# Kernel optimization log

Hardware: AMD Instinct MI355X
Metric: run time of the kernel (lower is better)

The kernel has to match this reference:

```python
import jax, jax.numpy as jnp
import numpy as np

N_NODES = 100000
N_EDGES = 1600000
IN_C = 64
OUT_C = 64


def setup_inputs() -> dict:
    key = jax.random.key(0)
    k1, k2, k3, k4, k5, k6 = jax.random.split(key, 6)
    x = jax.random.normal(k1, (N_NODES, IN_C), dtype=jnp.float32)
    column_index = jax.random.randint(k2, (N_EDGES,), 0, N_NODES, dtype=jnp.int32)
    row_index = jnp.sort(jax.random.randint(k3, (N_EDGES,), 0, N_NODES, dtype=jnp.int32))
    degrees = jax.random.uniform(k4, (N_NODES,), dtype=jnp.float32)
    # glorot (xavier_uniform) weight init, zero bias, matching reset_parameters()
    limit = np.sqrt(6.0 / (IN_C + OUT_C)).astype(np.float32)
    weight = jax.random.uniform(k5, (IN_C, OUT_C), dtype=jnp.float32, minval=-limit, maxval=limit)
    bias = jnp.zeros((OUT_C,), dtype=jnp.float32)
    return {"x": x, "weight": weight, "bias": bias, "column_index": column_index,
            "row_index": row_index, "degrees": degrees}


def reference(x, weight, bias, column_index, row_index, degrees):
    # GCN: transform then normalized neighbor aggregation (GNNAdvisor / ROF math).
    h = x @ weight                               # [N, out_c]
    gathered = h[column_index]                   # [E, out_c] gather source features
    agg = jax.ops.segment_sum(gathered, row_index, num_segments=N_NODES)  # [N, out_c]
    out = agg * degrees[:, None] + bias          # per-dst degree norm + bias
    return out
```

## Files before the change

kernel.cpp:

```cpp
#include <hip/hip_runtime.h>
#include <hip/hip_bf16.h>

#define IN_C 64
#define OUT_C 64

typedef __attribute__((ext_vector_type(8))) short bf16x8;
typedef __attribute__((ext_vector_type(4))) float f32x4;

__device__ __forceinline__ short f2bf(float f) {
    unsigned u = __float_as_uint(f);
    unsigned r = (u + 0x7FFFu + ((u >> 16) & 1u)) >> 16;
    return (short)r;
}

__global__ __launch_bounds__(256) void gcn_prep_kernel(
    const float* __restrict__ x, const float* __restrict__ w,
    unsigned short* __restrict__ h,
    const int* __restrict__ row, int* __restrict__ rowptr,
    int n_nodes, int n_edges, int gemm_blocks) {
    if ((int)blockIdx.x < gemm_blocks) {
        __shared__ bf16x8 wlds[512];
        const int tid  = threadIdx.x;
        const int lane = tid & 63;
        const int wv   = tid >> 6;
        const int m    = lane & 15;
        const int g    = lane >> 4;

        #pragma unroll
        for (int i = tid; i < IN_C * OUT_C; i += 256) {
            const int k = i >> 6, c = i & 63;
            const int ks = k >> 5, gg = (k >> 3) & 3, j = k & 7;
            const int nt = c >> 4, mm = c & 15;
            ((short*)wlds)[((ks * 4 + nt) * 64 + gg * 16 + mm) * 8 + j] =
                f2bf(w[i]);
        }
        __syncthreads();

        const int node0 = ((int)blockIdx.x * 4 + wv) * 16;
        if (node0 >= n_nodes) return;

        bf16x8 bfr[2][4];
        #pragma unroll
        for (int ks = 0; ks < 2; ++ks) {
            #pragma unroll
            for (int nt = 0; nt < 4; ++nt) {
                bfr[ks][nt] = wlds[(ks * 4 + nt) * 64 + g * 16 + m];
            }
        }

        const int arow = min(node0 + m, n_nodes - 1);
        const float* xr = x + (size_t)arow * IN_C;
        bf16x8 afr[2];
        #pragma unroll
        for (int ks = 0; ks < 2; ++ks) {
            const float4 p0 = *(const float4*)(xr + ks * 32 + g * 8);
            const float4 p1 = *(const float4*)(xr + ks * 32 + g * 8 + 4);
            union { short s[8]; bf16x8 v; } u;
            u.s[0] = f2bf(p0.x); u.s[1] = f2bf(p0.y);
            u.s[2] = f2bf(p0.z); u.s[3] = f2bf(p0.w);
            u.s[4] = f2bf(p1.x); u.s[5] = f2bf(p1.y);
            u.s[6] = f2bf(p1.z); u.s[7] = f2bf(p1.w);
            afr[ks] = u.v;
        }

        f32x4 acc[4];
        #pragma unroll
        for (int nt = 0; nt < 4; ++nt) acc[nt] = (f32x4){0.f, 0.f, 0.f, 0.f};
        #pragma unroll
        for (int ks = 0; ks < 2; ++ks) {
            #pragma unroll
            for (int nt = 0; nt < 4; ++nt) {
                acc[nt] = __builtin_amdgcn_mfma_f32_16x16x32_bf16(
                    afr[ks], bfr[ks][nt], acc[nt], 0, 0, 0);
            }
        }

        #pragma unroll
        for (int j = 0; j < 4; ++j) {
            const int node = node0 + g * 4 + j;
            if (node < n_nodes) {
                #pragma unroll
                for (int nt = 0; nt < 4; ++nt) {
                    h[(size_t)node * OUT_C + nt * 16 + m] =
                        (unsigned short)f2bf(acc[nt][j]);
                }
            }
        }
    } else {
        const int t  = ((int)blockIdx.x - gemm_blocks) * 256 + threadIdx.x;
        const int e0 = t * 4;
        if (e0 >= n_edges) return;
        const int4 r4 = *(const int4*)(row + e0);
        int rprev = (e0 == 0) ? -1 : row[e0 - 1];
        int rr[4] = {r4.x, r4.y, r4.z, r4.w};
        #pragma unroll
        for (int i = 0; i < 4; ++i) {
            if (e0 + i < n_edges) {
                for (int n = rprev + 1; n <= rr[i]; ++n) rowptr[n] = e0 + i;
                rprev = rr[i];
            }
        }
        if (e0 + 4 >= n_edges) {
            for (int n = rprev + 1; n <= n_nodes; ++n) rowptr[n] = n_edges;
        }
    }
}

#define UNPACK_ADD(v)                                   \
    do {                                                \
        acc[0] += __uint_as_float((v).x << 16);         \
        acc[1] += __uint_as_float((v).x & 0xFFFF0000u); \
        acc[2] += __uint_as_float((v).y << 16);         \
        acc[3] += __uint_as_float((v).y & 0xFFFF0000u); \
        acc[4] += __uint_as_float((v).z << 16);         \
        acc[5] += __uint_as_float((v).z & 0xFFFF0000u); \
        acc[6] += __uint_as_float((v).w << 16);         \
        acc[7] += __uint_as_float((v).w & 0xFFFF0000u); \
    } while (0)

__global__ __launch_bounds__(256) void gcn_agg_kernel(
    const uint4* __restrict__ h4, const int* __restrict__ col,
    const int* __restrict__ rowptr, const float* __restrict__ deg,
    const float4* __restrict__ bias4, float4* __restrict__ out4,
    int n_nodes) {
    const int tid  = threadIdx.x;
    const int node = blockIdx.x * 32 + (tid >> 3);
    if (node >= n_nodes) return;
    const int lo   = tid & 7;

    const int begin = rowptr[node];
    const int end   = rowptr[node + 1];
    const int last  = end - 1;

    float acc[8] = {0.f, 0.f, 0.f, 0.f, 0.f, 0.f, 0.f, 0.f};
    for (int e = begin; e < end; e += 8) {
        int c[8];
        #pragma unroll
        for (int i = 0; i < 8; ++i) c[i] = col[min(e + i, last)];
        uint4 v[8];
        #pragma unroll
        for (int i = 0; i < 8; ++i) v[i] = h4[(size_t)c[i] * 8 + lo];
        UNPACK_ADD(v[0]);
        #pragma unroll
        for (int i = 1; i < 8; ++i) {
            if (e + i <= last) UNPACK_ADD(v[i]);
        }
    }

    const float  d  = deg[node];
    const float4 b0 = bias4[lo * 2];
    const float4 b1 = bias4[lo * 2 + 1];
    float4 oa, ob;
    oa.x = fmaf(acc[0], d, b0.x);
    oa.y = fmaf(acc[1], d, b0.y);
    oa.z = fmaf(acc[2], d, b0.z);
    oa.w = fmaf(acc[3], d, b0.w);
    ob.x = fmaf(acc[4], d, b1.x);
    ob.y = fmaf(acc[5], d, b1.y);
    ob.z = fmaf(acc[6], d, b1.z);
    ob.w = fmaf(acc[7], d, b1.w);
    out4[(size_t)node * 16 + lo * 2]     = oa;
    out4[(size_t)node * 16 + lo * 2 + 1] = ob;
}

extern "C" void kernel_launch(void* const* d_in, const int* in_sizes, int n_in,
                              void* d_out, int out_size, void* d_ws, size_t ws_size,
                              hipStream_t stream) {
    const float* x    = (const float*)d_in[0];
    const float* w    = (const float*)d_in[1];
    const float* bias = (const float*)d_in[2];
    const int* col    = (const int*)d_in[3];
    const int* row    = (const int*)d_in[4];
    const float* deg  = (const float*)d_in[5];

    const int n_nodes = in_sizes[5];
    const int n_edges = in_sizes[3];

    unsigned short* h = (unsigned short*)d_ws;
    int* rowptr = (int*)((char*)d_ws +
                         (size_t)n_nodes * OUT_C * sizeof(unsigned short));

    const int gemm_blocks   = (n_nodes + 63) / 64;
    const int rowptr_blocks = (n_edges + 1023) / 1024;
    gcn_prep_kernel<<<gemm_blocks + rowptr_blocks, 256, 0, stream>>>(
        x, w, h, row, rowptr, n_nodes, n_edges, gemm_blocks);

    const int agg_blocks = (n_nodes + 31) / 32;
    gcn_agg_kernel<<<agg_blocks, 256, 0, stream>>>(
        (const uint4*)h, col, rowptr, deg,
        (const float4*)bias, (float4*)d_out, n_nodes);
}
```

Measured before the change: 126.9 us.

## Fuse prep and aggregation into one persistent cooperative kernel with grid sync

Replaces the two-launch sequence (GEMM plus rowptr build, then aggregation) with a single persistent cooperative kernel. It loops over the prep tiles, performs a grid-wide barrier, then loops over the aggregation blocks. Each block stages the weights into LDS once, and the change removes one kernel launch and the gap between kernels. In exchange it caps the grid at 2048 resident blocks, pays the cost of a grid sync and a per-call occupancy query, and falls back to the old two-kernel path if the cooperative launch fails.

```diff
diff --git a/kernel.cpp b/kernel.cpp
--- a/kernel.cpp
+++ b/kernel.cpp
@@ -1,5 +1,7 @@
 #include <hip/hip_runtime.h>
-#include <hip/hip_bf16.h>
+#include <hip/hip_cooperative_groups.h>
+
+namespace cg = cooperative_groups;
 
 #define IN_C 64
 #define OUT_C 64
@@ -11,99 +13,6 @@
     unsigned u = __float_as_uint(f);
     unsigned r = (u + 0x7FFFu + ((u >> 16) & 1u)) >> 16;
     return (short)r;
-}
-
-__global__ __launch_bounds__(256) void gcn_prep_kernel(
-    const float* __restrict__ x, const float* __restrict__ w,
-    unsigned short* __restrict__ h,
-    const int* __restrict__ row, int* __restrict__ rowptr,
-    int n_nodes, int n_edges, int gemm_blocks) {
-    if ((int)blockIdx.x < gemm_blocks) {
-        __shared__ bf16x8 wlds[512];
-        const int tid  = threadIdx.x;
-        const int lane = tid & 63;
-        const int wv   = tid >> 6;
-        const int m    = lane & 15;
-        const int g    = lane >> 4;
-
-        #pragma unroll
-        for (int i = tid; i < IN_C * OUT_C; i += 256) {
-            const int k = i >> 6, c = i & 63;
-            const int ks = k >> 5, gg = (k >> 3) & 3, j = k & 7;
-            const int nt = c >> 4, mm = c & 15;
-            ((short*)wlds)[((ks * 4 + nt) * 64 + gg * 16 + mm) * 8 + j] =
-                f2bf(w[i]);
-        }
-        __syncthreads();
-
-        const int node0 = ((int)blockIdx.x * 4 + wv) * 16;
-        if (node0 >= n_nodes) return;
-
-        bf16x8 bfr[2][4];
-        #pragma unroll
-        for (int ks = 0; ks < 2; ++ks) {
-            #pragma unroll
-            for (int nt = 0; nt < 4; ++nt) {
-                bfr[ks][nt] = wlds[(ks * 4 + nt) * 64 + g * 16 + m];
-            }
-        }
-
-        const int arow = min(node0 + m, n_nodes - 1);
-        const float* xr = x + (size_t)arow * IN_C;
-        bf16x8 afr[2];
-        #pragma unroll
-        for (int ks = 0; ks < 2; ++ks) {
-            const float4 p0 = *(const float4*)(xr + ks * 32 + g * 8);
-            const float4 p1 = *(const float4*)(xr + ks * 32 + g * 8 + 4);
-            union { short s[8]; bf16x8 v; } u;
-            u.s[0] = f2bf(p0.x); u.s[1] = f2bf(p0.y);
-            u.s[2] = f2bf(p0.z); u.s[3] = f2bf(p0.w);
-            u.s[4] = f2bf(p1.x); u.s[5] = f2bf(p1.y);
-            u.s[6] = f2bf(p1.z); u.s[7] = f2bf(p1.w);
-            afr[ks] = u.v;
-        }
-
-        f32x4 acc[4];
-        #pragma unroll
-        for (int nt = 0; nt < 4; ++nt) acc[nt] = (f32x4){0.f, 0.f, 0.f, 0.f};
-        #pragma unroll
-        for (int ks = 0; ks < 2; ++ks) {
-            #pragma unroll
-            for (int nt = 0; nt < 4; ++nt) {
-                acc[nt] = __builtin_amdgcn_mfma_f32_16x16x32_bf16(
-                    afr[ks], bfr[ks][nt], acc[nt], 0, 0, 0);
-            }
-        }
-
-        #pragma unroll
-        for (int j = 0; j < 4; ++j) {
-            const int node = node0 + g * 4 + j;
-            if (node < n_nodes) {
-                #pragma unroll
-                for (int nt = 0; nt < 4; ++nt) {
-                    h[(size_t)node * OUT_C + nt * 16 + m] =
-                        (unsigned short)f2bf(acc[nt][j]);
-                }
-            }
-        }
-    } else {
-        const int t  = ((int)blockIdx.x - gemm_blocks) * 256 + threadIdx.x;
-        const int e0 = t * 4;
-        if (e0 >= n_edges) return;
-        const int4 r4 = *(const int4*)(row + e0);
-        int rprev = (e0 == 0) ? -1 : row[e0 - 1];
-        int rr[4] = {r4.x, r4.y, r4.z, r4.w};
-        #pragma unroll
-        for (int i = 0; i < 4; ++i) {
-            if (e0 + i < n_edges) {
-                for (int n = rprev + 1; n <= rr[i]; ++n) rowptr[n] = e0 + i;
-                rprev = rr[i];
-            }
-        }
-        if (e0 + 4 >= n_edges) {
-            for (int n = rprev + 1; n <= n_nodes; ++n) rowptr[n] = n_edges;
-        }
-    }
 }
 
 #define UNPACK_ADD(v)                                   \
@@ -118,16 +27,90 @@
         acc[7] += __uint_as_float((v).w & 0xFFFF0000u); \
     } while (0)
 
-__global__ __launch_bounds__(256) void gcn_agg_kernel(
+
+__device__ __forceinline__ void gemm_tile_body(
+    const float* __restrict__ x, unsigned short* __restrict__ h,
+    int n_nodes, int tile, const bf16x8 bfr[2][4], int m, int g) {
+    const int node0 = tile * 16;
+    if (node0 >= n_nodes) return;
+
+    const int arow = min(node0 + m, n_nodes - 1);
+    const float* xr = x + (size_t)arow * IN_C;
+    bf16x8 afr[2];
+    #pragma unroll
+    for (int ks = 0; ks < 2; ++ks) {
+        const float4 p0 = *(const float4*)(xr + ks * 32 + g * 8);
+        const float4 p1 = *(const float4*)(xr + ks * 32 + g * 8 + 4);
+        union { short s[8]; bf16x8 v; } u;
+        u.s[0] = f2bf(p0.x); u.s[1] = f2bf(p0.y);
+        u.s[2] = f2bf(p0.z); u.s[3] = f2bf(p0.w);
+        u.s[4] = f2bf(p1.x); u.s[5] = f2bf(p1.y);
+        u.s[6] = f2bf(p1.z); u.s[7] = f2bf(p1.w);
+        afr[ks] = u.v;
+    }
+
+    f32x4 acc[4];
+    #pragma unroll
+    for (int nt = 0; nt < 4; ++nt) acc[nt] = (f32x4){0.f, 0.f, 0.f, 0.f};
+    #pragma unroll
+    for (int ks = 0; ks < 2; ++ks) {
+        #pragma unroll
+        for (int nt = 0; nt < 4; ++nt) {
+            acc[nt] = __builtin_amdgcn_mfma_f32_16x16x32_bf16(
+                afr[ks], bfr[ks][nt], acc[nt], 0, 0, 0);
+        }
+    }
+
+    #pragma unroll
+    for (int j = 0; j < 4; ++j) {
+        const int node = node0 + g * 4 + j;
+        if (node < n_nodes) {
+            #pragma unroll
+            for (int nt = 0; nt < 4; ++nt) {
+                h[(size_t)node * OUT_C + nt * 16 + m] =
+                    (unsigned short)f2bf(acc[nt][j]);
+            }
+        }
+    }
+}
+
+__device__ __forceinline__ void stage_w_body(
+    const float* __restrict__ w, bf16x8* wlds, int tid) {
+    #pragma unroll
+    for (int i = tid; i < IN_C * OUT_C; i += 256) {
+        const int k = i >> 6, c = i & 63;
+        const int ks = k >> 5, gg = (k >> 3) & 3, j = k & 7;
+        const int nt = c >> 4, mm = c & 15;
+        ((short*)wlds)[((ks * 4 + nt) * 64 + gg * 16 + mm) * 8 + j] =
+            f2bf(w[i]);
+    }
+}
+
+__device__ __forceinline__ void rowptr_body(
+    const int* __restrict__ row, int* __restrict__ rowptr,
+    int n_nodes, int n_edges, int t) {
+    const int e0 = t * 4;
+    if (e0 >= n_edges) return;
+    const int4 r4 = *(const int4*)(row + e0);
+    int rprev = (e0 == 0) ? -1 : row[e0 - 1];
+    int rr[4] = {r4.x, r4.y, r4.z, r4.w};
+    #pragma unroll
+    for (int i = 0; i < 4; ++i) {
+        if (e0 + i < n_edges) {
+            for (int n = rprev + 1; n <= rr[i]; ++n) rowptr[n] = e0 + i;
+            rprev = rr[i];
+        }
+    }
+    if (e0 + 4 >= n_edges) {
+        for (int n = rprev + 1; n <= n_nodes; ++n) rowptr[n] = n_edges;
+    }
+}
+
+__device__ __forceinline__ void agg_body(
     const uint4* __restrict__ h4, const int* __restrict__ col,
     const int* __restrict__ rowptr, const float* __restrict__ deg,
     const float4* __restrict__ bias4, float4* __restrict__ out4,
-    int n_nodes) {
-    const int tid  = threadIdx.x;
-    const int node = blockIdx.x * 32 + (tid >> 3);
-    if (node >= n_nodes) return;
-    const int lo   = tid & 7;
-
+    int node, int lo) {
     const int begin = rowptr[node];
     const int end   = rowptr[node + 1];
     const int last  = end - 1;
@@ -163,15 +146,104 @@
     out4[(size_t)node * 16 + lo * 2 + 1] = ob;
 }
 
+__global__ __launch_bounds__(256, 4) void gcn_fused_kernel(
+    const float* __restrict__ x, const float* __restrict__ w,
+    const int* __restrict__ row, const int* __restrict__ col,
+    const float* __restrict__ deg, const float4* __restrict__ bias4,
+    unsigned short* __restrict__ h, int* __restrict__ rowptr,
+    float4* __restrict__ out4,
+    int n_nodes, int n_edges,
+    int gemm_blocks, int rowptr_blocks, int agg_blocks, int nblocks) {
+    __shared__ bf16x8 wlds[512];
+    const int tid  = threadIdx.x;
+    const int lane = tid & 63;
+    const int wv   = tid >> 6;
+    const int m    = lane & 15;
+    const int g    = lane >> 4;
+
+    stage_w_body(w, wlds, tid);
+    __syncthreads();
+
+    bf16x8 bfr[2][4];
+    #pragma unroll
+    for (int ks = 0; ks < 2; ++ks) {
+        #pragma unroll
+        for (int nt = 0; nt < 4; ++nt) {
+            bfr[ks][nt] = wlds[(ks * 4 + nt) * 64 + g * 16 + m];
+        }
+    }
+
+    const int p1 = gemm_blocks + rowptr_blocks;
+    for (int b = blockIdx.x; b < p1; b += nblocks) {
+        if (b < gemm_blocks) {
+            gemm_tile_body(x, h, n_nodes, b * 4 + wv, bfr, m, g);
+        } else {
+            rowptr_body(row, rowptr, n_nodes, n_edges,
+                        (b - gemm_blocks) * 256 + tid);
+        }
+    }
+
+    cg::this_grid().sync();
+
+    const uint4* h4 = (const uint4*)h;
+    const int lo = tid & 7;
+    for (int b = blockIdx.x; b < agg_blocks; b += nblocks) {
+        const int node = b * 32 + (tid >> 3);
+        if (node < n_nodes) {
+            agg_body(h4, col, rowptr, deg, bias4, out4, node, lo);
+        }
+    }
+}
+
+__global__ __launch_bounds__(256) void gcn_prep_kernel(
+    const float* __restrict__ x, const float* __restrict__ w,
+    unsigned short* __restrict__ h,
+    const int* __restrict__ row, int* __restrict__ rowptr,
+    int n_nodes, int n_edges, int gemm_blocks) {
+    if ((int)blockIdx.x < gemm_blocks) {
+        __shared__ bf16x8 wlds[512];
+        const int tid  = threadIdx.x;
+        const int lane = tid & 63;
+        const int wv   = tid >> 6;
+        const int m    = lane & 15;
+        const int g    = lane >> 4;
+        stage_w_body(w, wlds, tid);
+        __syncthreads();
+        bf16x8 bfr[2][4];
+        #pragma unroll
+        for (int ks = 0; ks < 2; ++ks) {
+            #pragma unroll
+            for (int nt = 0; nt < 4; ++nt) {
+                bfr[ks][nt] = wlds[(ks * 4 + nt) * 64 + g * 16 + m];
+            }
+        }
+        gemm_tile_body(x, h, n_nodes, (int)blockIdx.x * 4 + wv, bfr, m, g);
+    } else {
+        rowptr_body(row, rowptr, n_nodes, n_edges,
+                    ((int)blockIdx.x - gemm_blocks) * 256 + threadIdx.x);
+    }
+}
+
+__global__ __launch_bounds__(256) void gcn_agg_kernel(
+    const uint4* __restrict__ h4, const int* __restrict__ col,
+    const int* __restrict__ rowptr, const float* __restrict__ deg,
+    const float4* __restrict__ bias4, float4* __restrict__ out4,
+    int n_nodes) {
+    const int node = blockIdx.x * 32 + (threadIdx.x >> 3);
+    if (node >= n_nodes) return;
+    agg_body(h4, col, rowptr, deg, bias4, out4, node, threadIdx.x & 7);
+}
+
 extern "C" void kernel_launch(void* const* d_in, const int* in_sizes, int n_in,
                               void* d_out, int out_size, void* d_ws, size_t ws_size,
                               hipStream_t stream) {
     const float* x    = (const float*)d_in[0];
     const float* w    = (const float*)d_in[1];
-    const float* bias = (const float*)d_in[2];
+    const float4* bias4 = (const float4*)d_in[2];
     const int* col    = (const int*)d_in[3];
     const int* row    = (const int*)d_in[4];
     const float* deg  = (const float*)d_in[5];
+    float4* out4      = (float4*)d_out;
 
     const int n_nodes = in_sizes[5];
     const int n_edges = in_sizes[3];
@@ -180,13 +252,29 @@
     int* rowptr = (int*)((char*)d_ws +
                          (size_t)n_nodes * OUT_C * sizeof(unsigned short));
 
-    const int gemm_blocks   = (n_nodes + 63) / 64;
-    const int rowptr_blocks = (n_edges + 1023) / 1024;
+    int gemm_blocks   = (n_nodes + 63) / 64;
+    int rowptr_blocks = (n_edges + 1023) / 1024;
+    int agg_blocks    = (n_nodes + 31) / 32;
+
+    int maxb = 0;
+    hipError_t qerr = hipOccupancyMaxActiveBlocksPerMultiprocessor(
+        &maxb, gcn_fused_kernel, 256, 0);
+    if (qerr == hipSuccess && maxb > 0) {
+        int nblocks = maxb * 256;
+        if (nblocks > 2048) nblocks = 2048;
+        void* args[] = {
+            (void*)&x, (void*)&w, (void*)&row, (void*)&col, (void*)&deg,
+            (void*)&bias4, (void*)&h, (void*)&rowptr, (void*)&out4,
+            (void*)&n_nodes, (void*)&n_edges,
+            (void*)&gemm_blocks, (void*)&rowptr_blocks, (void*)&agg_blocks,
+            (void*)&nblocks};
+        hipError_t lerr = hipLaunchCooperativeKernel(
+            gcn_fused_kernel, dim3(nblocks), dim3(256), args, 0u, stream);
+        if (lerr == hipSuccess) return;
+    }
+
     gcn_prep_kernel<<<gemm_blocks + rowptr_blocks, 256, 0, stream>>>(
         x, w, h, row, rowptr, n_nodes, n_edges, gemm_blocks);
-
-    const int agg_blocks = (n_nodes + 31) / 32;
     gcn_agg_kernel<<<agg_blocks, 256, 0, stream>>>(
-        (const uint4*)h, col, rowptr, deg,
-        (const float4*)bias, (float4*)d_out, n_nodes);
-}
+        (const uint4*)h, col, rowptr, deg, bias4, out4, n_nodes);
+}
```

Measured after the change: 214.3 us. 1.69x slower.
